# Kernel optimization log

Measured on AMD Instinct MI355X. Metric: run time of the kernel, lower is better.

The kernel has to match this reference:

```python
import jax, jax.numpy as jnp
import numpy as np

H = 128          # hidden_size
T, B = 2048, 128 # (seq_len, batch) -- nn.LSTM default batch_first=False
EPS = 1e-5       # BatchNorm1d eps


def setup_inputs() -> dict:
    key = jax.random.key(0)
    ks = jax.random.split(key, 16)
    s = 1.0 / np.sqrt(H)
    u = lambda k, shape: jax.random.uniform(k, shape, jnp.float32, -s, s)
    return {
        "x": jax.random.normal(ks[0], (T, B, 1), jnp.float32),
        # LSTM layer 0 (gate order i,f,g,o as in PyTorch)
        "Wih0": u(ks[1], (4 * H, 1)), "Whh0": u(ks[2], (4 * H, H)),
        "bih0": u(ks[3], (4 * H,)),   "bhh0": u(ks[4], (4 * H,)),
        # LSTM layer 1
        "Wih1": u(ks[5], (4 * H, H)), "Whh1": u(ks[6], (4 * H, H)),
        "bih1": u(ks[7], (4 * H,)),   "bhh1": u(ks[8], (4 * H,)),
        # head: Linear(128,128) -> BatchNorm1d(128) -> ReLU -> Linear(128,8)
        "fc1_w": u(ks[9], (H, H)), "fc1_b": u(ks[10], (H,)),
        "bn_gamma": jnp.ones((H,), jnp.float32),
        "bn_beta": jnp.zeros((H,), jnp.float32),
        "fc2_w": u(ks[11], (8, H)), "fc2_b": u(ks[12], (8,)),
    }


def _lstm_layer(x, Wih, Whh, bih, bhh):
    # x: (T, B, in) -> hidden states (T, B, H)
    h0 = jnp.zeros((x.shape[1], H), x.dtype)
    c0 = h0
    b = bih + bhh

    def step(carry, xt):
        h, c = carry
        g = xt @ Wih.T + h @ Whh.T + b        # (B, 4H)
        i, f, gg, o = jnp.split(g, 4, axis=-1)
        c = jax.nn.sigmoid(f) * c + jax.nn.sigmoid(i) * jnp.tanh(gg)
        h = jax.nn.sigmoid(o) * jnp.tanh(c)
        return (h, c), h

    _, hs = jax.lax.scan(step, (h0, c0), x)
    return hs


def reference(x, Wih0, Whh0, bih0, bhh0, Wih1, Whh1, bih1, bhh1,
              fc1_w, fc1_b, bn_gamma, bn_beta, fc2_w, fc2_b):
    h1 = _lstm_layer(x, Wih0, Whh0, bih0, bhh0)   # (T, B, H)
    h2 = _lstm_layer(h1, Wih1, Whh1, bih1, bhh1)  # (T, B, H)
    # Faithful to `x[:, -1, :]` with batch_first=False: last batch element, all timesteps
    y = h2[:, -1, :]                              # (T, H)
    z = y @ fc1_w.T + fc1_b                       # (T, H)
    # BatchNorm1d in training mode: batch stats over axis 0, biased variance
    mu = jnp.mean(z, axis=0)
    var = jnp.var(z, axis=0)
    z = (z - mu) * jax.lax.rsqrt(var + EPS) * bn_gamma + bn_beta
    z = jax.nn.relu(z)
    return z @ fc2_w.T + fc2_b                    # (T, 8)
```

## Files before the change

kernel.cpp:

```cpp
#include <hip/hip_runtime.h>
#include <math.h>

#define T_STEPS 2048
#define HID     128
#define G4      512
#define CH      16
#define NCHUNK  (T_STEPS / CH)

typedef _Float16 half8 __attribute__((ext_vector_type(8)));
typedef float    f32x4 __attribute__((ext_vector_type(4)));

__device__ __forceinline__ float fast_sig(float x) {
    return __fdividef(1.0f, 1.0f + __expf(-x));
}
__device__ __forceinline__ float fast_tanh(float x) {
    return fmaf(2.0f, __fdividef(1.0f, 1.0f + __expf(-2.0f * x)), -1.0f);
}

__global__ __launch_bounds__(256)
void lstm_pipe(const float* __restrict__ Whh0,
               const float* __restrict__ Whh1,
               const float* __restrict__ Wih1,
               const float* __restrict__ x,
               const float* __restrict__ wih0,
               const float* __restrict__ bih0,
               const float* __restrict__ bhh0,
               const float* __restrict__ bih1,
               const float* __restrict__ bhh1,
               unsigned int* __restrict__ flags,
               _Float16* __restrict__ h1h,
               float* __restrict__ hout2)
{
    const int tid  = threadIdx.x;
    const int wave = tid >> 6;
    const int lane = tid & 63;
    const int quad = lane >> 4;
    const int col  = lane & 15;
    const bool isL0 = (blockIdx.x == 0);

    const bool act_lane = (col < 8);
    const int  hh = (col >> 2) & 1;
    const int  rr = col & 3;
    const int  u  = wave * 32 + hh * 16 + quad * 4 + rr;

    __shared__ __align__(16) _Float16 h16[2][HID];
    __shared__ __align__(16) _Float16 h1s[2][CH][136];
    __shared__ __align__(16) float    Gbuf[2][CH][516];
    __shared__ float x_s[T_STEPS];

    const float* Whh = isL0 ? Whh0 : Whh1;
    half8 afrag[8][4];
    #pragma unroll
    for (int r = 0; r < 8; ++r) {
        const float* row = Whh +
            (size_t)(128 * (r >> 1) + wave * 32 + (r & 1) * 16 + col) * HID;
        #pragma unroll
        for (int kt = 0; kt < 4; ++kt) {
            const float4* p = reinterpret_cast<const float4*>(row + kt * 32 + quad * 8);
            float4 lo = p[0], hi = p[1];
            half8 h;
            h[0] = (_Float16)lo.x; h[1] = (_Float16)lo.y;
            h[2] = (_Float16)lo.z; h[3] = (_Float16)lo.w;
            h[4] = (_Float16)hi.x; h[5] = (_Float16)hi.y;
            h[6] = (_Float16)hi.z; h[7] = (_Float16)hi.w;
            afrag[r][kt] = h;
        }
    }
    #pragma unroll
    for (int r = 0; r < 8; ++r)
        #pragma unroll
        for (int kt = 0; kt < 4; ++kt) asm volatile("" : "+a"(afrag[r][kt]));

    f32x4 bsum4 = {0,0,0,0}, w4 = {0,0,0,0};
    if (act_lane) {
        #pragma unroll
        for (int g = 0; g < 4; ++g) {
            if (isL0) {
                bsum4[g] = bih0[128 * g + u] + bhh0[128 * g + u];
                w4[g]    = wih0[128 * g + u];
            } else {
                bsum4[g] = bih1[128 * g + u] + bhh1[128 * g + u];
            }
        }
    }
    asm volatile("" : "+v"(bsum4), "+v"(w4));

    if (isL0) {
        for (int i = tid; i < T_STEPS; i += 256)
            x_s[i] = x[(size_t)i * HID + HID - 1];
    }

    if (tid < HID) h16[0][tid] = (_Float16)0.0f;
    __syncthreads();

    float c_reg = 0.0f;
    const f32x4 zero4 = {0.f, 0.f, 0.f, 0.f};

    if (isL0) {
        for (int t = 0; t < T_STEPS; ++t) {
            half8 b0 = *reinterpret_cast<const half8*>(&h16[t & 1][ 0 + quad * 8]);
            half8 b1 = *reinterpret_cast<const half8*>(&h16[t & 1][32 + quad * 8]);
            half8 b2 = *reinterpret_cast<const half8*>(&h16[t & 1][64 + quad * 8]);
            half8 b3 = *reinterpret_cast<const half8*>(&h16[t & 1][96 + quad * 8]);

            f32x4 acc[8];
            #pragma unroll
            for (int r = 0; r < 8; ++r)
                acc[r] = __builtin_amdgcn_mfma_f32_16x16x32_f16(afrag[r][0], b0, zero4, 0, 0, 0);
            #pragma unroll
            for (int r = 0; r < 8; ++r)
                acc[r] = __builtin_amdgcn_mfma_f32_16x16x32_f16(afrag[r][1], b1, acc[r], 0, 0, 0);
            #pragma unroll
            for (int r = 0; r < 8; ++r)
                acc[r] = __builtin_amdgcn_mfma_f32_16x16x32_f16(afrag[r][2], b2, acc[r], 0, 0, 0);
            #pragma unroll
            for (int r = 0; r < 8; ++r)
                acc[r] = __builtin_amdgcn_mfma_f32_16x16x32_f16(afrag[r][3], b3, acc[r], 0, 0, 0);

            float gi = 0.f, gf = 0.f, gg = 0.f, go = 0.f;
            #pragma unroll
            for (int cs = 0; cs < 8; ++cs) {
                if (col == cs) {
                    const int h2_ = cs >> 2, r2_ = cs & 3;
                    gi = acc[0 + h2_][r2_];
                    gf = acc[2 + h2_][r2_];
                    gg = acc[4 + h2_][r2_];
                    go = acc[6 + h2_][r2_];
                }
            }
            f32x4 pre = bsum4 + w4 * x_s[t];
            gi += pre[0]; gf += pre[1]; gg += pre[2]; go += pre[3];

            const float ai = fast_sig(gi);
            const float af = fast_sig(gf);
            const float ag = fast_tanh(gg);
            const float ao = fast_sig(go);
            c_reg = fmaf(af, c_reg, ai * ag);
            const float h = ao * fast_tanh(c_reg);

            if (act_lane) {
                const _Float16 hf = (_Float16)h;
                h16[(t + 1) & 1][u] = hf;
                h1h[(size_t)t * HID + u] = hf;
            }
            __syncthreads();

            if ((t & 15) == 15 && tid == 0)
                __hip_atomic_store(&flags[t >> 4], 1u,
                                   __ATOMIC_RELEASE, __HIP_MEMORY_SCOPE_AGENT);
        }
    } else {
        half8 wfrag[8][4];
        #pragma unroll
        for (int mt = 0; mt < 8; ++mt) {
            const float* row = Wih1 + (size_t)((wave * 8 + mt) * 16 + col) * HID;
            #pragma unroll
            for (int kt = 0; kt < 4; ++kt) {
                const float4* p = reinterpret_cast<const float4*>(row + kt * 32 + quad * 8);
                float4 lo = p[0], hi = p[1];
                half8 h;
                h[0] = (_Float16)lo.x; h[1] = (_Float16)lo.y;
                h[2] = (_Float16)lo.z; h[3] = (_Float16)lo.w;
                h[4] = (_Float16)hi.x; h[5] = (_Float16)hi.y;
                h[6] = (_Float16)hi.z; h[7] = (_Float16)hi.w;
                wfrag[mt][kt] = h;
            }
        }
        #pragma unroll
        for (int mt = 0; mt < 8; ++mt)
            #pragma unroll
            for (int kt = 0; kt < 4; ++kt) asm volatile("" : "+a"(wfrag[mt][kt]));

        if (lane == 0) {
            while (__hip_atomic_load(&flags[0],
                       __ATOMIC_ACQUIRE, __HIP_MEMORY_SCOPE_AGENT) == 0u)
                __builtin_amdgcn_s_sleep(2);
        }
        {
            const int row = tid >> 4, c16 = tid & 15;
            half8 v = *reinterpret_cast<const half8*>(
                h1h + (size_t)row * HID + c16 * 8);
            *reinterpret_cast<half8*>(&h1s[0][row][c16 * 8]) = v;
        }
        __syncthreads();
        #pragma unroll
        for (int mt = 0; mt < 8; ++mt) {
            f32x4 ag = zero4;
            #pragma unroll
            for (int kt = 0; kt < 4; ++kt) {
                half8 bg = *reinterpret_cast<const half8*>(
                    &h1s[0][col][kt * 32 + quad * 8]);
                ag = __builtin_amdgcn_mfma_f32_16x16x32_f16(wfrag[mt][kt], bg, ag, 0, 0, 0);
            }
            *reinterpret_cast<float4*>(&Gbuf[0][col][(wave * 8 + mt) * 16 + quad * 4]) =
                make_float4(ag[0], ag[1], ag[2], ag[3]);
        }
        __syncthreads();

        for (int j = 0; j < T_STEPS; ++j) {
            const int p  = j & 15;
            const int ct = j >> 4;
            const int cn = ct + 1;

            if (p == 0 && cn < NCHUNK) {
                if (lane == 0) {
                    while (__hip_atomic_load(&flags[cn],
                               __ATOMIC_ACQUIRE, __HIP_MEMORY_SCOPE_AGENT) == 0u)
                        __builtin_amdgcn_s_sleep(2);
                }
                const int row = tid >> 4, c16 = tid & 15;
                half8 v = *reinterpret_cast<const half8*>(
                    h1h + (size_t)(cn * CH + row) * HID + c16 * 8);
                *reinterpret_cast<half8*>(&h1s[cn & 1][row][c16 * 8]) = v;
            }

            #pragma unroll
            for (int mt = 0; mt < 8; ++mt) {
                if (p == mt + 1 && cn < NCHUNK) {
                    f32x4 ag = zero4;
                    #pragma unroll
                    for (int kt = 0; kt < 4; ++kt) {
                        half8 bg = *reinterpret_cast<const half8*>(
                            &h1s[cn & 1][col][kt * 32 + quad * 8]);
                        ag = __builtin_amdgcn_mfma_f32_16x16x32_f16(wfrag[mt][kt], bg, ag, 0, 0, 0);
                    }
                    *reinterpret_cast<float4*>(
                        &Gbuf[cn & 1][col][(wave * 8 + mt) * 16 + quad * 4]) =
                        make_float4(ag[0], ag[1], ag[2], ag[3]);
                }
            }

            half8 b0 = *reinterpret_cast<const half8*>(&h16[j & 1][ 0 + quad * 8]);
            half8 b1 = *reinterpret_cast<const half8*>(&h16[j & 1][32 + quad * 8]);
            half8 b2 = *reinterpret_cast<const half8*>(&h16[j & 1][64 + quad * 8]);
            half8 b3 = *reinterpret_cast<const half8*>(&h16[j & 1][96 + quad * 8]);

            f32x4 pre = bsum4;
            if (act_lane) {
                const float* gr = &Gbuf[ct & 1][p][u];
                pre[0] += gr[0];
                pre[1] += gr[128];
                pre[2] += gr[256];
                pre[3] += gr[384];
            }

            f32x4 acc[8];
            #pragma unroll
            for (int r = 0; r < 8; ++r)
                acc[r] = __builtin_amdgcn_mfma_f32_16x16x32_f16(afrag[r][0], b0, zero4, 0, 0, 0);
            #pragma unroll
            for (int r = 0; r < 8; ++r)
                acc[r] = __builtin_amdgcn_mfma_f32_16x16x32_f16(afrag[r][1], b1, acc[r], 0, 0, 0);
            #pragma unroll
            for (int r = 0; r < 8; ++r)
                acc[r] = __builtin_amdgcn_mfma_f32_16x16x32_f16(afrag[r][2], b2, acc[r], 0, 0, 0);
            #pragma unroll
            for (int r = 0; r < 8; ++r)
                acc[r] = __builtin_amdgcn_mfma_f32_16x16x32_f16(afrag[r][3], b3, acc[r], 0, 0, 0);

            float gi = 0.f, gf = 0.f, gg = 0.f, go = 0.f;
            #pragma unroll
            for (int cs = 0; cs < 8; ++cs) {
                if (col == cs) {
                    const int h2_ = cs >> 2, r2_ = cs & 3;
                    gi = acc[0 + h2_][r2_];
                    gf = acc[2 + h2_][r2_];
                    gg = acc[4 + h2_][r2_];
                    go = acc[6 + h2_][r2_];
                }
            }
            gi += pre[0]; gf += pre[1]; gg += pre[2]; go += pre[3];

            const float ai = fast_sig(gi);
            const float af = fast_sig(gf);
            const float ag = fast_tanh(gg);
            const float ao = fast_sig(go);
            c_reg = fmaf(af, c_reg, ai * ag);
            const float h = ao * fast_tanh(c_reg);

            if (act_lane) {
                h16[(j + 1) & 1][u] = (_Float16)h;
                hout2[(size_t)j * HID + u] = h;
            }
            __syncthreads();
        }
    }
}

#define BM 64
#define BN 64
__global__ __launch_bounds__(256)
void gemm_bias_kernel(const float* __restrict__ A,
                      const float* __restrict__ W,
                      const float* __restrict__ b1,
                      const float* __restrict__ b2,
                      float* __restrict__ C,
                      int M, int N)
{
    __shared__ float Al[128][BM + 4];
    __shared__ float Wl[128][BN + 4];
    const int tid    = threadIdx.x;
    const int m_base = blockIdx.x * BM;
    const int n_base = blockIdx.y * BN;

    {
        const int r  = tid >> 2;
        const int kq = (tid & 3) * 32;
        const float4* srcA = reinterpret_cast<const float4*>(A + (size_t)(m_base + r) * 128 + kq);
        #pragma unroll
        for (int i = 0; i < 8; ++i) {
            float4 v = srcA[i];
            int k = kq + 4 * i;
            Al[k + 0][r] = v.x; Al[k + 1][r] = v.y; Al[k + 2][r] = v.z; Al[k + 3][r] = v.w;
        }
        const float4* srcW = reinterpret_cast<const float4*>(W + (size_t)(n_base + r) * 128 + kq);
        #pragma unroll
        for (int i = 0; i < 8; ++i) {
            float4 v = srcW[i];
            int k = kq + 4 * i;
            Wl[k + 0][r] = v.x; Wl[k + 1][r] = v.y; Wl[k + 2][r] = v.z; Wl[k + 3][r] = v.w;
        }
    }
    __syncthreads();

    const int tm = (tid & 15) * 4;
    const int tn = (tid >> 4) * 4;
    float acc[4][4] = {};
    #pragma unroll 8
    for (int k = 0; k < 128; ++k) {
        float4 av = *reinterpret_cast<const float4*>(&Al[k][tm]);
        float4 wv = *reinterpret_cast<const float4*>(&Wl[k][tn]);
        acc[0][0] = fmaf(av.x, wv.x, acc[0][0]);
        acc[0][1] = fmaf(av.x, wv.y, acc[0][1]);
        acc[0][2] = fmaf(av.x, wv.z, acc[0][2]);
        acc[0][3] = fmaf(av.x, wv.w, acc[0][3]);
        acc[1][0] = fmaf(av.y, wv.x, acc[1][0]);
        acc[1][1] = fmaf(av.y, wv.y, acc[1][1]);
        acc[1][2] = fmaf(av.y, wv.z, acc[1][2]);
        acc[1][3] = fmaf(av.y, wv.w, acc[1][3]);
        acc[2][0] = fmaf(av.z, wv.x, acc[2][0]);
        acc[2][1] = fmaf(av.z, wv.y, acc[2][1]);
        acc[2][2] = fmaf(av.z, wv.z, acc[2][2]);
        acc[2][3] = fmaf(av.z, wv.w, acc[2][3]);
        acc[3][0] = fmaf(av.w, wv.x, acc[3][0]);
        acc[3][1] = fmaf(av.w, wv.y, acc[3][1]);
        acc[3][2] = fmaf(av.w, wv.z, acc[3][2]);
        acc[3][3] = fmaf(av.w, wv.w, acc[3][3]);
    }

    float bias[4];
    #pragma unroll
    for (int i = 0; i < 4; ++i) {
        int n = n_base + tn + i;
        bias[i] = b1[n] + (b2 ? b2[n] : 0.0f);
    }
    #pragma unroll
    for (int mi = 0; mi < 4; ++mi) {
        float4 o;
        o.x = acc[mi][0] + bias[0];
        o.y = acc[mi][1] + bias[1];
        o.z = acc[mi][2] + bias[2];
        o.w = acc[mi][3] + bias[3];
        *reinterpret_cast<float4*>(C + (size_t)(m_base + tm + mi) * N + n_base + tn) = o;
    }
}

__global__ __launch_bounds__(512)
void bn_stats_kernel(const float* __restrict__ Z,
                     const float* __restrict__ gamma,
                     const float* __restrict__ beta,
                     float* __restrict__ scale,
                     float* __restrict__ shift)
{
    const int tid = threadIdx.x;
    const int col = tid & 127;
    const int seg = tid >> 7;
    float s = 0.f, sq = 0.f;
    for (int t = seg * 512; t < (seg + 1) * 512; ++t) {
        float v = Z[(size_t)t * 128 + col];
        s += v;
        sq = fmaf(v, v, sq);
    }
    __shared__ float ps[4][128], pq[4][128];
    ps[seg][col] = s;
    pq[seg][col] = sq;
    __syncthreads();
    if (tid < 128) {
        float sum = ps[0][tid] + ps[1][tid] + ps[2][tid] + ps[3][tid];
        float sqq = pq[0][tid] + pq[1][tid] + pq[2][tid] + pq[3][tid];
        float mean = sum * (1.0f / 2048.0f);
        float var  = sqq * (1.0f / 2048.0f) - mean * mean;
        float sc = gamma[tid] * rsqrtf(var + 1e-5f);
        scale[tid] = sc;
        shift[tid] = beta[tid] - mean * sc;
    }
}

__global__ __launch_bounds__(512)
void fc2_kernel(const float* __restrict__ Z,
                const float* __restrict__ scale,
                const float* __restrict__ shift,
                const float* __restrict__ fc2_w,
                const float* __restrict__ fc2_b,
                float* __restrict__ out)
{
    const int gid = blockIdx.x * blockDim.x + threadIdx.x;
    const int o = gid & 7;
    const int t = gid >> 3;

    __shared__ float w_s[8][132];
    __shared__ float sc_s[128], sh_s[128];
    for (int i = threadIdx.x; i < 1024; i += 512) w_s[i >> 7][i & 127] = fc2_w[i];
    if (threadIdx.x < 128) {
        sc_s[threadIdx.x] = scale[threadIdx.x];
        sh_s[threadIdx.x] = shift[threadIdx.x];
    }
    __syncthreads();

    float acc = fc2_b[o];
    const float* zrow = Z + (size_t)t * 128;
    #pragma unroll 4
    for (int k = 0; k < 128; ++k) {
        float zn = fmaf(zrow[k], sc_s[k], sh_s[k]);
        zn = fmaxf(zn, 0.0f);
        acc = fmaf(zn, w_s[o][k], acc);
    }
    out[gid] = acc;
}

extern "C" void kernel_launch(void* const* d_in, const int* in_sizes, int n_in,
                              void* d_out, int out_size, void* d_ws, size_t ws_size,
                              hipStream_t stream)
{
    const float* x     = (const float*)d_in[0];
    const float* Wih0  = (const float*)d_in[1];
    const float* Whh0  = (const float*)d_in[2];
    const float* bih0  = (const float*)d_in[3];
    const float* bhh0  = (const float*)d_in[4];
    const float* Wih1  = (const float*)d_in[5];
    const float* Whh1  = (const float*)d_in[6];
    const float* bih1  = (const float*)d_in[7];
    const float* bhh1  = (const float*)d_in[8];
    const float* fc1_w = (const float*)d_in[9];
    const float* fc1_b = (const float*)d_in[10];
    const float* gamma = (const float*)d_in[11];
    const float* beta  = (const float*)d_in[12];
    const float* fc2_w = (const float*)d_in[13];
    const float* fc2_b = (const float*)d_in[14];
    float* out = (float*)d_out;

    unsigned int* flags = (unsigned int*)d_ws;
    _Float16* h1h  = (_Float16*)((char*)d_ws + 1024);
    float*    h2   = (float*)((char*)d_ws + 1024 + T_STEPS * HID * 2);
    float*    z    = h2 + T_STEPS * HID;
    float*    scale= z  + T_STEPS * HID;
    float*    shift= scale + 128;

    hipMemsetAsync(flags, 0, 1024, stream);

    lstm_pipe<<<2, 256, 0, stream>>>(Whh0, Whh1, Wih1, x, Wih0,
                                     bih0, bhh0, bih1, bhh1,
                                     flags, h1h, h2);

    dim3 g4(T_STEPS / BM, HID / BN);
    gemm_bias_kernel<<<g4, 256, 0, stream>>>(h2, fc1_w, fc1_b, nullptr, z, T_STEPS, HID);

    bn_stats_kernel<<<1, 512, 0, stream>>>(z, gamma, beta, scale, shift);

    fc2_kernel<<<T_STEPS * 8 / 512, 512, 0, stream>>>(z, scale, shift, fc2_w, fc2_b, out);
}
```

Baseline: 2.229 ms.

## Split layer-1 input projection into a third producer block via global G buffer

Adds a third workgroup that computes the layer-1 input projection (Wih1·h1) chunk by chunk and writes it to a global G buffer. It signals each chunk through a second flag array. This takes the interleaved MFMA projection work off the layer-1 recurrent block's serial critical path, and that block now just prefetches its precomputed gate inputs one step ahead. A large shared-memory pad forces each block onto its own CU, at the cost of extra global traffic and another cross-block synchronisation stage.

```diff
diff --git a/kernel.cpp b/kernel.cpp
--- a/kernel.cpp
+++ b/kernel.cpp
@@ -18,25 +18,27 @@
 }
 
 __global__ __launch_bounds__(256)
-void lstm_pipe(const float* __restrict__ Whh0,
-               const float* __restrict__ Whh1,
-               const float* __restrict__ Wih1,
-               const float* __restrict__ x,
-               const float* __restrict__ wih0,
-               const float* __restrict__ bih0,
-               const float* __restrict__ bhh0,
-               const float* __restrict__ bih1,
-               const float* __restrict__ bhh1,
-               unsigned int* __restrict__ flags,
-               _Float16* __restrict__ h1h,
-               float* __restrict__ hout2)
+void lstm_pipe3(const float* __restrict__ Whh0,
+                const float* __restrict__ Whh1,
+                const float* __restrict__ Wih1,
+                const float* __restrict__ x,
+                const float* __restrict__ wih0,
+                const float* __restrict__ bih0,
+                const float* __restrict__ bhh0,
+                const float* __restrict__ bih1,
+                const float* __restrict__ bhh1,
+                unsigned int* __restrict__ flags1,
+                unsigned int* __restrict__ flags2,
+                _Float16* __restrict__ h1h,
+                float* __restrict__ G,
+                float* __restrict__ hout2)
 {
     const int tid  = threadIdx.x;
     const int wave = tid >> 6;
     const int lane = tid & 63;
     const int quad = lane >> 4;
     const int col  = lane & 15;
-    const bool isL0 = (blockIdx.x == 0);
+    const int bid  = blockIdx.x;
 
     const bool act_lane = (col < 8);
     const int  hh = (col >> 2) & 1;
@@ -44,10 +46,70 @@
     const int  u  = wave * 32 + hh * 16 + quad * 4 + rr;
 
     __shared__ __align__(16) _Float16 h16[2][HID];
-    __shared__ __align__(16) _Float16 h1s[2][CH][136];
-    __shared__ __align__(16) float    Gbuf[2][CH][516];
+    __shared__ __align__(16) _Float16 h1s[CH][136];
     __shared__ float x_s[T_STEPS];
-
+    __shared__ char occupancy_pad[70400];
+    ((volatile char*)occupancy_pad)[tid] = 0;
+
+    const f32x4 zero4 = {0.f, 0.f, 0.f, 0.f};
+
+    if (bid == 1) {
+        half8 wfrag[8][4];
+        #pragma unroll
+        for (int mt = 0; mt < 8; ++mt) {
+            const float* row = Wih1 + (size_t)((wave * 8 + mt) * 16 + col) * HID;
+            #pragma unroll
+            for (int kt = 0; kt < 4; ++kt) {
+                const float4* p = reinterpret_cast<const float4*>(row + kt * 32 + quad * 8);
+                float4 lo = p[0], hi = p[1];
+                half8 h;
+                h[0] = (_Float16)lo.x; h[1] = (_Float16)lo.y;
+                h[2] = (_Float16)lo.z; h[3] = (_Float16)lo.w;
+                h[4] = (_Float16)hi.x; h[5] = (_Float16)hi.y;
+                h[6] = (_Float16)hi.z; h[7] = (_Float16)hi.w;
+                wfrag[mt][kt] = h;
+            }
+        }
+        #pragma unroll
+        for (int mt = 0; mt < 8; ++mt)
+            #pragma unroll
+            for (int kt = 0; kt < 4; ++kt) asm volatile("" : "+a"(wfrag[mt][kt]));
+
+        for (int c = 0; c < NCHUNK; ++c) {
+            if (lane == 0) {
+                while (__hip_atomic_load(&flags1[c],
+                           __ATOMIC_ACQUIRE, __HIP_MEMORY_SCOPE_AGENT) == 0u)
+                    __builtin_amdgcn_s_sleep(8);
+            }
+            {
+                const int row = tid >> 4, c16 = tid & 15;
+                half8 v = *reinterpret_cast<const half8*>(
+                    h1h + (size_t)(c * CH + row) * HID + c16 * 8);
+                *reinterpret_cast<half8*>(&h1s[row][c16 * 8]) = v;
+            }
+            __syncthreads();
+            #pragma unroll
+            for (int mt = 0; mt < 8; ++mt) {
+                f32x4 ag = zero4;
+                #pragma unroll
+                for (int kt = 0; kt < 4; ++kt) {
+                    half8 bg = *reinterpret_cast<const half8*>(
+                        &h1s[col][kt * 32 + quad * 8]);
+                    ag = __builtin_amdgcn_mfma_f32_16x16x32_f16(wfrag[mt][kt], bg, ag, 0, 0, 0);
+                }
+                *reinterpret_cast<float4*>(
+                    &G[(size_t)(c * CH + col) * G4 + (wave * 8 + mt) * 16 + quad * 4]) =
+                    make_float4(ag[0], ag[1], ag[2], ag[3]);
+            }
+            __syncthreads();
+            if (tid == 0)
+                __hip_atomic_store(&flags2[c], 1u,
+                                   __ATOMIC_RELEASE, __HIP_MEMORY_SCOPE_AGENT);
+        }
+        return;
+    }
+
+    const bool isL0 = (bid == 0);
     const float* Whh = isL0 ? Whh0 : Whh1;
     half8 afrag[8][4];
     #pragma unroll
@@ -94,7 +156,6 @@
     __syncthreads();
 
     float c_reg = 0.0f;
-    const f32x4 zero4 = {0.f, 0.f, 0.f, 0.f};
 
     if (isL0) {
         for (int t = 0; t < T_STEPS; ++t) {
@@ -146,103 +207,44 @@
             __syncthreads();
 
             if ((t & 15) == 15 && tid == 0)
-                __hip_atomic_store(&flags[t >> 4], 1u,
+                __hip_atomic_store(&flags1[t >> 4], 1u,
                                    __ATOMIC_RELEASE, __HIP_MEMORY_SCOPE_AGENT);
         }
     } else {
-        half8 wfrag[8][4];
-        #pragma unroll
-        for (int mt = 0; mt < 8; ++mt) {
-            const float* row = Wih1 + (size_t)((wave * 8 + mt) * 16 + col) * HID;
-            #pragma unroll
-            for (int kt = 0; kt < 4; ++kt) {
-                const float4* p = reinterpret_cast<const float4*>(row + kt * 32 + quad * 8);
-                float4 lo = p[0], hi = p[1];
-                half8 h;
-                h[0] = (_Float16)lo.x; h[1] = (_Float16)lo.y;
-                h[2] = (_Float16)lo.z; h[3] = (_Float16)lo.w;
-                h[4] = (_Float16)hi.x; h[5] = (_Float16)hi.y;
-                h[6] = (_Float16)hi.z; h[7] = (_Float16)hi.w;
-                wfrag[mt][kt] = h;
-            }
-        }
-        #pragma unroll
-        for (int mt = 0; mt < 8; ++mt)
-            #pragma unroll
-            for (int kt = 0; kt < 4; ++kt) asm volatile("" : "+a"(wfrag[mt][kt]));
-
         if (lane == 0) {
-            while (__hip_atomic_load(&flags[0],
+            while (__hip_atomic_load(&flags2[0],
                        __ATOMIC_ACQUIRE, __HIP_MEMORY_SCOPE_AGENT) == 0u)
-                __builtin_amdgcn_s_sleep(2);
-        }
-        {
-            const int row = tid >> 4, c16 = tid & 15;
-            half8 v = *reinterpret_cast<const half8*>(
-                h1h + (size_t)row * HID + c16 * 8);
-            *reinterpret_cast<half8*>(&h1s[0][row][c16 * 8]) = v;
-        }
-        __syncthreads();
-        #pragma unroll
-        for (int mt = 0; mt < 8; ++mt) {
-            f32x4 ag = zero4;
-            #pragma unroll
-            for (int kt = 0; kt < 4; ++kt) {
-                half8 bg = *reinterpret_cast<const half8*>(
-                    &h1s[0][col][kt * 32 + quad * 8]);
-                ag = __builtin_amdgcn_mfma_f32_16x16x32_f16(wfrag[mt][kt], bg, ag, 0, 0, 0);
-            }
-            *reinterpret_cast<float4*>(&Gbuf[0][col][(wave * 8 + mt) * 16 + quad * 4]) =
-                make_float4(ag[0], ag[1], ag[2], ag[3]);
-        }
-        __syncthreads();
-
-        for (int j = 0; j < T_STEPS; ++j) {
-            const int p  = j & 15;
-            const int ct = j >> 4;
-            const int cn = ct + 1;
-
-            if (p == 0 && cn < NCHUNK) {
+                __builtin_amdgcn_s_sleep(8);
+        }
+        f32x4 pre_cur = {0,0,0,0}, pre_nxt = {0,0,0,0};
+        if (act_lane) {
+            #pragma unroll
+            for (int g = 0; g < 4; ++g)
+                pre_cur[g] = G[128 * g + u];
+        }
+
+        for (int t = 0; t < T_STEPS; ++t) {
+            if (((t + 1) & 15) == 0 && (t + 1) < T_STEPS) {
+                const int cn = (t + 1) >> 4;
                 if (lane == 0) {
-                    while (__hip_atomic_load(&flags[cn],
+                    while (__hip_atomic_load(&flags2[cn],
                                __ATOMIC_ACQUIRE, __HIP_MEMORY_SCOPE_AGENT) == 0u)
-                        __builtin_amdgcn_s_sleep(2);
+                        __builtin_amdgcn_s_sleep(8);
                 }
-                const int row = tid >> 4, c16 = tid & 15;
-                half8 v = *reinterpret_cast<const half8*>(
-                    h1h + (size_t)(cn * CH + row) * HID + c16 * 8);
-                *reinterpret_cast<half8*>(&h1s[cn & 1][row][c16 * 8]) = v;
-            }
-
-            #pragma unroll
-            for (int mt = 0; mt < 8; ++mt) {
-                if (p == mt + 1 && cn < NCHUNK) {
-                    f32x4 ag = zero4;
-                    #pragma unroll
-                    for (int kt = 0; kt < 4; ++kt) {
-                        half8 bg = *reinterpret_cast<const half8*>(
-                            &h1s[cn & 1][col][kt * 32 + quad * 8]);
-                        ag = __builtin_amdgcn_mfma_f32_16x16x32_f16(wfrag[mt][kt], bg, ag, 0, 0, 0);
-                    }
-                    *reinterpret_cast<float4*>(
-                        &Gbuf[cn & 1][col][(wave * 8 + mt) * 16 + quad * 4]) =
-                        make_float4(ag[0], ag[1], ag[2], ag[3]);
-                }
-            }
-
-            half8 b0 = *reinterpret_cast<const half8*>(&h16[j & 1][ 0 + quad * 8]);
-            half8 b1 = *reinterpret_cast<const half8*>(&h16[j & 1][32 + quad * 8]);
-            half8 b2 = *reinterpret_cast<const half8*>(&h16[j & 1][64 + quad * 8]);
-            half8 b3 = *reinterpret_cast<const half8*>(&h16[j & 1][96 + quad * 8]);
-
-            f32x4 pre = bsum4;
+            }
+
+            half8 b0 = *reinterpret_cast<const half8*>(&h16[t & 1][ 0 + quad * 8]);
+            half8 b1 = *reinterpret_cast<const half8*>(&h16[t & 1][32 + quad * 8]);
+            half8 b2 = *reinterpret_cast<const half8*>(&h16[t & 1][64 + quad * 8]);
+            half8 b3 = *reinterpret_cast<const half8*>(&h16[t & 1][96 + quad * 8]);
+
+            const int tn = (t + 1 < T_STEPS) ? t + 1 : t;
             if (act_lane) {
-                const float* gr = &Gbuf[ct & 1][p][u];
-                pre[0] += gr[0];
-                pre[1] += gr[128];
-                pre[2] += gr[256];
-                pre[3] += gr[384];
-            }
+                #pragma unroll
+                for (int g = 0; g < 4; ++g)
+                    pre_nxt[g] = G[(size_t)tn * G4 + 128 * g + u];
+            }
+            asm volatile("" : "+v"(pre_nxt));
 
             f32x4 acc[8];
             #pragma unroll
@@ -269,7 +271,10 @@
                     go = acc[6 + h2_][r2_];
                 }
             }
-            gi += pre[0]; gf += pre[1]; gg += pre[2]; go += pre[3];
+            gi += pre_cur[0] + bsum4[0];
+            gf += pre_cur[1] + bsum4[1];
+            gg += pre_cur[2] + bsum4[2];
+            go += pre_cur[3] + bsum4[3];
 
             const float ai = fast_sig(gi);
             const float af = fast_sig(gf);
@@ -279,9 +284,10 @@
             const float h = ao * fast_tanh(c_reg);
 
             if (act_lane) {
-                h16[(j + 1) & 1][u] = (_Float16)h;
-                hout2[(size_t)j * HID + u] = h;
-            }
+                h16[(t + 1) & 1][u] = (_Float16)h;
+                hout2[(size_t)t * HID + u] = h;
+            }
+            pre_cur = pre_nxt;
             __syncthreads();
         }
     }
@@ -449,18 +455,20 @@
     const float* fc2_b = (const float*)d_in[14];
     float* out = (float*)d_out;
 
-    unsigned int* flags = (unsigned int*)d_ws;
-    _Float16* h1h  = (_Float16*)((char*)d_ws + 1024);
-    float*    h2   = (float*)((char*)d_ws + 1024 + T_STEPS * HID * 2);
+    unsigned int* flags1 = (unsigned int*)d_ws;
+    unsigned int* flags2 = flags1 + 256;
+    _Float16* h1h  = (_Float16*)((char*)d_ws + 2048);
+    float*    G    = (float*)((char*)d_ws + 2048 + T_STEPS * HID * 2);
+    float*    h2   = G + (size_t)T_STEPS * G4;
     float*    z    = h2 + T_STEPS * HID;
     float*    scale= z  + T_STEPS * HID;
     float*    shift= scale + 128;
 
-    hipMemsetAsync(flags, 0, 1024, stream);
-
-    lstm_pipe<<<2, 256, 0, stream>>>(Whh0, Whh1, Wih1, x, Wih0,
-                                     bih0, bhh0, bih1, bhh1,
-                                     flags, h1h, h2);
+    hipMemsetAsync(flags1, 0, 2048, stream);
+
+    lstm_pipe3<<<3, 256, 0, stream>>>(Whh0, Whh1, Wih1, x, Wih0,
+                                      bih0, bhh0, bih1, bhh1,
+                                      flags1, flags2, h1h, G, h2);
 
     dim3 g4(T_STEPS / BM, HID / BN);
     gemm_bias_kernel<<<g4, 256, 0, stream>>>(h2, fc1_w, fc1_b, nullptr, z, T_STEPS, HID);
```

Result: faster. 2.110 ms (-5.3%).
